# Kernel optimization log

Hardware: AMD Instinct MI355X
Metric: run time of the kernel (lower is better)

Reference implementation:

```python
import jax, jax.numpy as jnp
import numpy as np

NE = 8192       # number of mesh elements
B = 64          # batch of density fields
AVG_DEG = 32    # neighbors per element within filter radius
NNZ = NE * AVG_DEG
NEG_SLOPE = 0.001


def setup_inputs() -> dict:
    key = jax.random.key(0)
    kx, kw, ks, ki = jax.random.split(key, 4)
    x = jax.random.normal(kx, (B, NE), dtype=jnp.float32)
    fc1_weight = jax.random.normal(kw, (NE, NE), dtype=jnp.float32) * (1.0 / np.sqrt(NE))
    # sparse weights initialized uniform(-bound, bound), bound = sqrt(2/Ne)
    bound = float(np.sqrt(2.0 / NE))
    sparse_weights = jax.random.uniform(ks, (NNZ,), dtype=jnp.float32,
                                        minval=-bound, maxval=bound)
    # static COO pattern (row, col) derived from mesh connectivity Rij < Rmin
    sparse_indices = jax.random.randint(ki, (2, NNZ), 0, NE, dtype=jnp.int64)
    return {"x": x, "fc1_weight": fc1_weight,
            "sparse_weights": sparse_weights, "sparse_indices": sparse_indices}


def reference(x, fc1_weight, sparse_weights, sparse_indices):
    # dense layer: h[b, i] = sum_k x[b, k] * W[i, k]
    h = x @ fc1_weight.T                         # [B, Ne]
    rows = sparse_indices[0]                     # [nnz]
    cols = sparse_indices[1]                     # [nnz]
    # sparse mm: out[b, j] = sum_{(i,j) in pattern} h[b, i] * w_{ij}
    contrib = h[:, rows] * sparse_weights        # [B, nnz] gather + scale
    out = jnp.zeros((x.shape[0], fc1_weight.shape[0]), dtype=h.dtype)
    out = out.at[:, cols].add(contrib)           # scatter-add over columns
    # leaky_relu, negative_slope = 0.001
    return jnp.where(out >= 0, out, NEG_SLOPE * out)
```

## Files before the change

### kernel.cpp

```cpp
#include <hip/hip_runtime.h>
#include <hip/hip_bf16.h>

#define NE 8192
#define BATCH 64
#define NNZT (NE * 32)
#define BK 64
#define SAK 72
#define TN 16

typedef float f32x4 __attribute__((ext_vector_type(4)));
typedef short s16x8 __attribute__((ext_vector_type(8)));

__device__ __forceinline__ unsigned short f2bf(float f) {
  unsigned u = __builtin_bit_cast(unsigned, f);
  return (unsigned short)((u + 0x7FFFu + ((u >> 16) & 1u)) >> 16);
}

__global__ void k_convert_x(const float* __restrict__ x, unsigned short* __restrict__ xb) {
  int i = (blockIdx.x * 256 + threadIdx.x) * 4;
  float4 v = *reinterpret_cast<const float4*>(x + i);
  *reinterpret_cast<ushort4*>(xb + i) =
      make_ushort4(f2bf(v.x), f2bf(v.y), f2bf(v.z), f2bf(v.w));
}

__global__ void k_zero(float* __restrict__ p) {
  int i = (blockIdx.x * 256 + threadIdx.x) * 4;
  *reinterpret_cast<float4*>(p + i) = make_float4(0.f, 0.f, 0.f, 0.f);
}

__global__ __launch_bounds__(256, 2) void k_gemm(const unsigned short* __restrict__ xb,
                                                 const float* __restrict__ W,
                                                 float* __restrict__ ht) {
  __shared__ __align__(16) unsigned short sA[BATCH * SAK];
  __shared__ __align__(16) unsigned short sB[TN * SAK];
  const int tid = threadIdx.x;
  const int i0 = blockIdx.x * TN;

  const int rA = tid >> 2, cA = (tid & 3) * 16;
  const int rB = tid >> 4, cB = (tid & 15) * 4;

  const unsigned short* xptr = xb + rA * NE + cA;
  const float* wptr = W + (size_t)(i0 + rB) * NE + cB;
  unsigned short* sAp = sA + rA * SAK + cA;
  unsigned short* sBp = sB + rB * SAK + cB;

  const int wave = tid >> 6, lane = tid & 63;
  const int lrow = lane & 15, kofs = (lane >> 4) * 8;
  const unsigned short* aRd = sA + (wave * 16 + lrow) * SAK + kofs;
  const unsigned short* bRd = sB + lrow * SAK + kofs;

  f32x4 acc = {0.f, 0.f, 0.f, 0.f};

  uint4 xr0 = *reinterpret_cast<const uint4*>(xptr);
  uint4 xr1 = *reinterpret_cast<const uint4*>(xptr + 8);
  float4 wr = *reinterpret_cast<const float4*>(wptr);

  for (int k0 = 0;;) {
    *reinterpret_cast<uint4*>(sAp) = xr0;
    *reinterpret_cast<uint4*>(sAp + 8) = xr1;
    *reinterpret_cast<ushort4*>(sBp) =
        make_ushort4(f2bf(wr.x), f2bf(wr.y), f2bf(wr.z), f2bf(wr.w));
    __syncthreads();
    k0 += BK;
    if (k0 < NE) {
      xr0 = *reinterpret_cast<const uint4*>(xptr + k0);
      xr1 = *reinterpret_cast<const uint4*>(xptr + k0 + 8);
      wr = *reinterpret_cast<const float4*>(wptr + k0);
    }
#pragma unroll
    for (int ks = 0; ks < 2; ++ks) {
      s16x8 bfr = *reinterpret_cast<const s16x8*>(bRd + ks * 32);
      s16x8 afr = *reinterpret_cast<const s16x8*>(aRd + ks * 32);
      acc = __builtin_amdgcn_mfma_f32_16x16x32_bf16(afr, bfr, acc, 0, 0, 0);
    }
    if (k0 >= NE) break;
    __syncthreads();
  }

  float* hp = ht + (size_t)(i0 + lrow) * BATCH + wave * 16 + (lane >> 4) * 4;
  *reinterpret_cast<f32x4*>(hp) = acc;
}

__global__ void k_scatter(const float* __restrict__ ht, const float* __restrict__ sw,
                          const int* __restrict__ rows, const int* __restrict__ cols,
                          float* __restrict__ out_t) {
  const int w = (blockIdx.x * 256 + threadIdx.x) >> 6;
  const int lane = threadIdx.x & 63;
  const int n0 = w * (NNZT / 4096);
#pragma unroll 4
  for (int n = n0; n < n0 + (NNZT / 4096); ++n) {
    const int r = rows[n];
    const int c = cols[n];
    const float wv = sw[n];
    atomicAdd(out_t + (size_t)c * BATCH + lane, ht[(size_t)r * BATCH + lane] * wv);
  }
}

__global__ void k_final(const float* __restrict__ out_t, float* __restrict__ out) {
  __shared__ float tile[64][65];
  const int t = threadIdx.x;
  const int j0 = blockIdx.x * 64;
  {
    const int jl = t >> 2, b0 = (t & 3) * 16;
    const float* src = out_t + (size_t)(j0 + jl) * BATCH + b0;
#pragma unroll
    for (int e = 0; e < 16; e += 4) {
      float4 v = *reinterpret_cast<const float4*>(src + e);
      tile[jl][b0 + e + 0] = v.x;
      tile[jl][b0 + e + 1] = v.y;
      tile[jl][b0 + e + 2] = v.z;
      tile[jl][b0 + e + 3] = v.w;
    }
  }
  __syncthreads();
  {
    const int bl = t >> 2, js = (t & 3) * 16;
    float* dst = out + (size_t)bl * NE + j0 + js;
#pragma unroll
    for (int e = 0; e < 16; e += 4) {
      float a0 = tile[js + e + 0][bl];
      float a1 = tile[js + e + 1][bl];
      float a2 = tile[js + e + 2][bl];
      float a3 = tile[js + e + 3][bl];
      float4 v;
      v.x = a0 >= 0.f ? a0 : 0.001f * a0;
      v.y = a1 >= 0.f ? a1 : 0.001f * a1;
      v.z = a2 >= 0.f ? a2 : 0.001f * a2;
      v.w = a3 >= 0.f ? a3 : 0.001f * a3;
      *reinterpret_cast<float4*>(dst + e) = v;
    }
  }
}

extern "C" void kernel_launch(void* const* d_in, const int* in_sizes, int n_in,
                              void* d_out, int out_size, void* d_ws, size_t ws_size,
                              hipStream_t stream) {
  const float* x = (const float*)d_in[0];
  const float* W = (const float*)d_in[1];
  const float* sw = (const float*)d_in[2];
  const int* idx = (const int*)d_in[3];
  float* out = (float*)d_out;

  char* ws = (char*)d_ws;
  float* ht = (float*)ws;
  unsigned short* xbf = (unsigned short*)(ws + (2 << 20));
  float* out_t = (float*)(ws + (3 << 20));

  k_convert_x<<<512, 256, 0, stream>>>(x, xbf);
  k_zero<<<512, 256, 0, stream>>>(out_t);
  k_gemm<<<512, 256, 0, stream>>>(xbf, W, ht);
  k_scatter<<<1024, 256, 0, stream>>>(ht, sw, idx, idx + NNZT, out_t);
  k_final<<<128, 256, 0, stream>>>(out_t, out);
}
```

Baseline: 163.5 us.

## Replace LDS-tiled GEMM with split-K register-direct MFMA and atomic reduction

The dense layer no longer stages tiles in shared memory with per-step barriers. Each wave now loads W and bf16 x fragments straight from global memory into registers and runs four MFMAs per step, reusing one converted W fragment across all 64 batch rows. K is split 8 ways over 4096 waves, and partial sums are reduced into a zeroed buffer with float atomics. This removes barrier and LDS overhead and raises parallelism, at the cost of redundant x loads, atomic traffic, and non-deterministic summation order.

```diff
diff --git a/kernel.cpp b/kernel.cpp
--- a/kernel.cpp
+++ b/kernel.cpp
@@ -4,9 +4,8 @@
 #define NE 8192
 #define BATCH 64
 #define NNZT (NE * 32)
-#define BK 64
-#define SAK 72
-#define TN 16
+#define KSPLIT 8
+#define KCH (NE / KSPLIT)
 
 typedef float f32x4 __attribute__((ext_vector_type(4)));
 typedef short s16x8 __attribute__((ext_vector_type(8)));
@@ -14,6 +13,16 @@
 __device__ __forceinline__ unsigned short f2bf(float f) {
   unsigned u = __builtin_bit_cast(unsigned, f);
   return (unsigned short)((u + 0x7FFFu + ((u >> 16) & 1u)) >> 16);
+}
+
+__device__ __forceinline__ s16x8 cvt8(f32x4 a, f32x4 b) {
+  s16x8 r;
+#pragma unroll
+  for (int j = 0; j < 4; ++j) {
+    r[j] = (short)f2bf(a[j]);
+    r[j + 4] = (short)f2bf(b[j]);
+  }
+  return r;
 }
 
 __global__ void k_convert_x(const float* __restrict__ x, unsigned short* __restrict__ xb) {
@@ -28,57 +37,48 @@
   *reinterpret_cast<float4*>(p + i) = make_float4(0.f, 0.f, 0.f, 0.f);
 }
 
-__global__ __launch_bounds__(256, 2) void k_gemm(const unsigned short* __restrict__ xb,
-                                                 const float* __restrict__ W,
-                                                 float* __restrict__ ht) {
-  __shared__ __align__(16) unsigned short sA[BATCH * SAK];
-  __shared__ __align__(16) unsigned short sB[TN * SAK];
-  const int tid = threadIdx.x;
-  const int i0 = blockIdx.x * TN;
+__global__ __launch_bounds__(256, 4) void k_dense(const unsigned short* __restrict__ xb,
+                                                  const float* __restrict__ W,
+                                                  float* __restrict__ ht) {
+  const int lane = threadIdx.x & 63;
+  const int gw = blockIdx.x * 4 + (threadIdx.x >> 6);
+  const int i0 = (gw >> 3) * 16;
+  const int kq = gw & 7;
+  const int row16 = lane & 15;
+  const int k8 = (lane >> 4) * 8;
 
-  const int rA = tid >> 2, cA = (tid & 3) * 16;
-  const int rB = tid >> 4, cB = (tid & 15) * 4;
+  const float* wp = W + (size_t)(i0 + row16) * NE + kq * KCH + k8;
+  const unsigned short* xp = xb + (size_t)row16 * NE + kq * KCH + k8;
 
-  const unsigned short* xptr = xb + rA * NE + cA;
-  const float* wptr = W + (size_t)(i0 + rB) * NE + cB;
-  unsigned short* sAp = sA + rA * SAK + cA;
-  unsigned short* sBp = sB + rB * SAK + cB;
+  f32x4 acc0 = {0.f, 0.f, 0.f, 0.f};
+  f32x4 acc1 = {0.f, 0.f, 0.f, 0.f};
+  f32x4 acc2 = {0.f, 0.f, 0.f, 0.f};
+  f32x4 acc3 = {0.f, 0.f, 0.f, 0.f};
 
-  const int wave = tid >> 6, lane = tid & 63;
-  const int lrow = lane & 15, kofs = (lane >> 4) * 8;
-  const unsigned short* aRd = sA + (wave * 16 + lrow) * SAK + kofs;
-  const unsigned short* bRd = sB + lrow * SAK + kofs;
-
-  f32x4 acc = {0.f, 0.f, 0.f, 0.f};
-
-  uint4 xr0 = *reinterpret_cast<const uint4*>(xptr);
-  uint4 xr1 = *reinterpret_cast<const uint4*>(xptr + 8);
-  float4 wr = *reinterpret_cast<const float4*>(wptr);
-
-  for (int k0 = 0;;) {
-    *reinterpret_cast<uint4*>(sAp) = xr0;
-    *reinterpret_cast<uint4*>(sAp + 8) = xr1;
-    *reinterpret_cast<ushort4*>(sBp) =
-        make_ushort4(f2bf(wr.x), f2bf(wr.y), f2bf(wr.z), f2bf(wr.w));
-    __syncthreads();
-    k0 += BK;
-    if (k0 < NE) {
-      xr0 = *reinterpret_cast<const uint4*>(xptr + k0);
-      xr1 = *reinterpret_cast<const uint4*>(xptr + k0 + 8);
-      wr = *reinterpret_cast<const float4*>(wptr + k0);
-    }
-#pragma unroll
-    for (int ks = 0; ks < 2; ++ks) {
-      s16x8 bfr = *reinterpret_cast<const s16x8*>(bRd + ks * 32);
-      s16x8 afr = *reinterpret_cast<const s16x8*>(aRd + ks * 32);
-      acc = __builtin_amdgcn_mfma_f32_16x16x32_bf16(afr, bfr, acc, 0, 0, 0);
-    }
-    if (k0 >= NE) break;
-    __syncthreads();
+#pragma unroll 2
+  for (int k = 0; k < KCH; k += 32) {
+    f32x4 w0 = *reinterpret_cast<const f32x4*>(wp + k);
+    f32x4 w1 = *reinterpret_cast<const f32x4*>(wp + k + 4);
+    s16x8 a0 = *reinterpret_cast<const s16x8*>(xp + k);
+    s16x8 a1 = *reinterpret_cast<const s16x8*>(xp + (size_t)16 * NE + k);
+    s16x8 a2 = *reinterpret_cast<const s16x8*>(xp + (size_t)32 * NE + k);
+    s16x8 a3 = *reinterpret_cast<const s16x8*>(xp + (size_t)48 * NE + k);
+    s16x8 bfr = cvt8(w0, w1);
+    acc0 = __builtin_amdgcn_mfma_f32_16x16x32_bf16(a0, bfr, acc0, 0, 0, 0);
+    acc1 = __builtin_amdgcn_mfma_f32_16x16x32_bf16(a1, bfr, acc1, 0, 0, 0);
+    acc2 = __builtin_amdgcn_mfma_f32_16x16x32_bf16(a2, bfr, acc2, 0, 0, 0);
+    acc3 = __builtin_amdgcn_mfma_f32_16x16x32_bf16(a3, bfr, acc3, 0, 0, 0);
   }
 
-  float* hp = ht + (size_t)(i0 + lrow) * BATCH + wave * 16 + (lane >> 4) * 4;
-  *reinterpret_cast<f32x4*>(hp) = acc;
+  float* hp = ht + (size_t)(i0 + row16) * BATCH + (lane >> 4) * 4;
+#pragma unroll
+  for (int j = 0; j < 4; ++j) atomicAdd(hp + j, acc0[j]);
+#pragma unroll
+  for (int j = 0; j < 4; ++j) atomicAdd(hp + 16 + j, acc1[j]);
+#pragma unroll
+  for (int j = 0; j < 4; ++j) atomicAdd(hp + 32 + j, acc2[j]);
+#pragma unroll
+  for (int j = 0; j < 4; ++j) atomicAdd(hp + 48 + j, acc3[j]);
 }
 
 __global__ void k_scatter(const float* __restrict__ ht, const float* __restrict__ sw,
@@ -143,12 +143,12 @@
 
   char* ws = (char*)d_ws;
   float* ht = (float*)ws;
-  unsigned short* xbf = (unsigned short*)(ws + (2 << 20));
-  float* out_t = (float*)(ws + (3 << 20));
+  float* out_t = (float*)(ws + (2 << 20));
+  unsigned short* xbf = (unsigned short*)(ws + (4 << 20));
 
   k_convert_x<<<512, 256, 0, stream>>>(x, xbf);
-  k_zero<<<512, 256, 0, stream>>>(out_t);
-  k_gemm<<<512, 256, 0, stream>>>(xbf, W, ht);
+  k_zero<<<1024, 256, 0, stream>>>((float*)ws);
+  k_dense<<<1024, 256, 0, stream>>>(xbf, W, ht);
   k_scatter<<<1024, 256, 0, stream>>>(ht, sw, idx, idx + NNZT, out_t);
   k_final<<<128, 256, 0, stream>>>(out_t, out);
 }
```

Result: slower. 206.6 us (+26.4%).
